# Kernel optimization log

Hardware: AMD Instinct MI355X
Metric: run time of the kernel (lower is better)

The kernel has to match this reference:

```python
import jax, jax.numpy as jnp
import numpy as np

NUM_EXPERT = 8
IN_FEAT = 1024
OUT_FEAT = 1024
N_TOKENS = 8192


def setup_inputs() -> dict:
    key = jax.random.key(0)
    k_inp, k_gate, k_w = jax.random.split(key, 3)
    inp = jax.random.normal(k_inp, (N_TOKENS, IN_FEAT), dtype=jnp.float32)
    gate = jax.random.randint(k_gate, (N_TOKENS,), 0, NUM_EXPERT, dtype=jnp.int32)
    # FMoELinear weight: [num_expert, out_feat, in_feat], kaiming-uniform-like init
    bound = 1.0 / np.sqrt(IN_FEAT)
    weight = jax.random.uniform(
        k_w, (NUM_EXPERT, OUT_FEAT, IN_FEAT), dtype=jnp.float32,
        minval=-bound, maxval=bound)
    return {"inp": inp, "gate": gate, "weight": weight}


def reference(inp, gate, weight):
    # out[i] = weight[gate[i]] @ inp[i]  (top-1 MoE dispatch + grouped GEMM + combine)
    # Loop over the small fixed expert set via scan; each step does a masked
    # dense GEMM so only tokens routed to expert e contribute.
    n, _ = inp.shape
    num_expert, out_feat, _ = weight.shape

    def body(acc, ew):
        e, w_e = ew  # w_e: [out_feat, in_feat]
        mask = (gate == e).astype(inp.dtype)[:, None]  # [n, 1]
        acc = acc + (inp * mask) @ w_e.T               # [n, out_feat]
        return acc, None

    init = jnp.zeros((n, out_feat), dtype=inp.dtype)
    out, _ = jax.lax.scan(body, init, (jnp.arange(num_expert), weight))
    return out
```

## Files before the change

### kernel.cpp

```cpp
#include <hip/hip_runtime.h>
#include <hip/hip_bf16.h>

#define N_TOKENS 8192
#define IN_FEAT 1024
#define OUT_FEAT 1024
#define NUM_EXPERT 8

#define BM 128
#define BN 128
#define BK 32
#define MAXT 71

typedef __bf16 bf16x8 __attribute__((ext_vector_type(8)));
typedef float f32x4 __attribute__((ext_vector_type(4)));

__device__ __forceinline__ unsigned int rne16(float x) {
    union { float f; unsigned int u; } c;
    c.f = x;
    unsigned int u = c.u;
    u += 0x7fffu + ((u >> 16) & 1u);
    return u >> 16;
}
__device__ __forceinline__ unsigned int pk2(float x, float y) {
    return rne16(x) | (rne16(y) << 16);
}

__device__ __forceinline__ void load_lds16(const void* g, void* l) {
    __builtin_amdgcn_global_load_lds(
        (const __attribute__((address_space(1))) unsigned int*)g,
        (__attribute__((address_space(3))) unsigned int*)l,
        16, 0, 0);
}


__global__ __launch_bounds__(256) void moe_hist(const int* __restrict__ gate,
                                                int* __restrict__ cnt) {
    __shared__ int lc[NUM_EXPERT];
    const int t = threadIdx.x;
    if (t < NUM_EXPERT) lc[t] = 0;
    __syncthreads();
    int g = gate[blockIdx.x * 256 + t];
    atomicAdd(&lc[g], 1);
    __syncthreads();
    if (t < NUM_EXPERT) atomicAdd(&cnt[t], lc[t]);
}

__global__ void moe_scan(const int* __restrict__ cnt, int* __restrict__ seg,
                         int* __restrict__ cur, int* __restrict__ tiles,
                         int* __restrict__ ntiles) {
    int s = 0;
    #pragma unroll
    for (int e = 0; e < NUM_EXPERT; ++e) { seg[e] = s; cur[e] = s; s += cnt[e]; }
    seg[NUM_EXPERT] = s;
    int T = 0;
    for (int e = 0; e < NUM_EXPERT; ++e) {
        int c = cnt[e], b = seg[e];
        for (int mt = 0; mt * BM < c; ++mt) {
            int rows = c - mt * BM; if (rows > BM) rows = BM;
            tiles[T++] = (b + mt * BM) | (e << 13) | (rows << 16);
        }
    }
    *ntiles = T;
}

__global__ __launch_bounds__(256) void moe_scatter(const int* __restrict__ gate,
                                                   int* __restrict__ cur,
                                                   int* __restrict__ perm) {
    const int t = threadIdx.x;
    const int lane = t & 63;
    const unsigned long long lt = (lane == 0) ? 0ull : (~0ull >> (64 - lane));
    const int i = blockIdx.x * 256 + t;
    int g = gate[i];
    #pragma unroll
    for (int e = 0; e < NUM_EXPERT; ++e) {
        unsigned long long m = __ballot(g == e);
        if (g == e) {
            int rank = __popcll(m & lt);
            int leader = (int)__ffsll((unsigned long long)m) - 1;
            int p0 = 0;
            if (rank == 0) p0 = atomicAdd(&cur[e], __popcll(m));
            p0 = __shfl(p0, leader);
            perm[p0 + rank] = i;
        }
    }
}

__global__ __launch_bounds__(256) void moe_prep(const float* __restrict__ inp,
                                                const float* __restrict__ weight,
                                                const int* __restrict__ perm,
                                                unsigned int* __restrict__ A2,
                                                unsigned int* __restrict__ W2) {
    const int bid = blockIdx.x;
    const int t = threadIdx.x;
    const int wave = t >> 6, lane = t & 63;
    const float* src;
    unsigned int* dst;
    if (bid < 2048) {
        int row = bid * 4 + wave;
        src = inp + perm[row] * IN_FEAT;
        dst = A2 + row * (IN_FEAT / 2);
    } else {
        int row = (bid - 2048) * 4 + wave;
        src = weight + row * IN_FEAT;
        dst = W2 + row * (IN_FEAT / 2);
    }
    #pragma unroll
    for (int j = 0; j < 4; ++j) {
        float4 v = *(const float4*)(src + j * 256 + lane * 4);
        uint2 o;
        o.x = pk2(v.x, v.y);
        o.y = pk2(v.z, v.w);
        *(uint2*)(dst + j * 128 + lane * 2) = o;
    }
}

__global__ __launch_bounds__(256, 4) void moe_gemm(
    const unsigned short* __restrict__ A2,
    const unsigned short* __restrict__ W2,
    const int* __restrict__ perm,
    const int* __restrict__ tiles,
    const int* __restrict__ ntiles,
    float* __restrict__ out) {

    const int bid = blockIdx.x;
    const int tIdx = bid >> 3;
    const int ntile = bid & 7;
    if (tIdx >= *ntiles) return;
    const int tile = tiles[tIdx];
    const int tbase = tile & 8191;
    const int e = (tile >> 13) & 7;
    const int rows = tile >> 16;

    __shared__ unsigned short lA[2][BM * BK];
    __shared__ unsigned short lB[2][BN * BK];
    __shared__ int rowids[BM];

    const int t = threadIdx.x;
    if (t < BM) {
        int r = tbase + t;
        rowids[t] = perm[r < N_TOKENS ? r : N_TOKENS - 1];
    }

    const int crow = t >> 2;
    const int p = (t & 3) ^ (crow & 3);
    int ar0 = tbase + crow;       if (ar0 > N_TOKENS - 1) ar0 = N_TOKENS - 1;
    int ar1 = tbase + 64 + crow;  if (ar1 > N_TOKENS - 1) ar1 = N_TOKENS - 1;
    const unsigned short* gA0 = A2 + ar0 * IN_FEAT + p * 8;
    const unsigned short* gA1 = A2 + ar1 * IN_FEAT + p * 8;
    const unsigned short* gB0 = W2 + e * (OUT_FEAT * IN_FEAT)
                                + (ntile * BN + crow) * IN_FEAT + p * 8;
    const unsigned short* gB1 = gB0 + 64 * IN_FEAT;
    const int dofs = t * 8;
    const int dofs2 = (t + 256) * 8;

    const int wave = t >> 6;
    const int lane = t & 63;
    const int wm = (wave & 1) << 6;
    const int wn = (wave >> 1) << 6;
    const int l15 = lane & 15;
    const int quad = lane >> 4;
    const int qx = quad ^ (l15 & 3);
    const int fofsA = (wm + l15) * BK + qx * 8;
    const int fofsB = (wn + l15) * BK + qx * 8;

    f32x4 acc[4][4];
    #pragma unroll
    for (int i = 0; i < 4; ++i)
        #pragma unroll
        for (int j = 0; j < 4; ++j)
            acc[i][j] = (f32x4)0.0f;

    load_lds16(gA0, &lA[0][dofs]);
    load_lds16(gA1, &lA[0][dofs2]);
    load_lds16(gB0, &lB[0][dofs]);
    load_lds16(gB1, &lB[0][dofs2]);

    #pragma unroll 1
    for (int kk = 0; kk < 16; ++kk) {
        const int k0 = kk * 64;

        __syncthreads();
        load_lds16(gA0 + k0 + 32, &lA[1][dofs]);
        load_lds16(gA1 + k0 + 32, &lA[1][dofs2]);
        load_lds16(gB0 + k0 + 32, &lB[1][dofs]);
        load_lds16(gB1 + k0 + 32, &lB[1][dofs2]);

        {
            bf16x8 af[4], bq[4];
            #pragma unroll
            for (int i = 0; i < 4; ++i)
                af[i] = *(const bf16x8*)&lA[0][fofsA + i * 16 * BK];
            #pragma unroll
            for (int j = 0; j < 4; ++j)
                bq[j] = *(const bf16x8*)&lB[0][fofsB + j * 16 * BK];
            #pragma unroll
            for (int i = 0; i < 4; ++i)
                #pragma unroll
                for (int j = 0; j < 4; ++j)
                    acc[i][j] = __builtin_amdgcn_mfma_f32_16x16x32_bf16(
                        af[i], bq[j], acc[i][j], 0, 0, 0);
        }

        __syncthreads();
        if (kk < 15) {
            load_lds16(gA0 + k0 + 64, &lA[0][dofs]);
            load_lds16(gA1 + k0 + 64, &lA[0][dofs2]);
            load_lds16(gB0 + k0 + 64, &lB[0][dofs]);
            load_lds16(gB1 + k0 + 64, &lB[0][dofs2]);
        }

        {
            bf16x8 af[4], bq[4];
            #pragma unroll
            for (int i = 0; i < 4; ++i)
                af[i] = *(const bf16x8*)&lA[1][fofsA + i * 16 * BK];
            #pragma unroll
            for (int j = 0; j < 4; ++j)
                bq[j] = *(const bf16x8*)&lB[1][fofsB + j * 16 * BK];
            #pragma unroll
            for (int i = 0; i < 4; ++i)
                #pragma unroll
                for (int j = 0; j < 4; ++j)
                    acc[i][j] = __builtin_amdgcn_mfma_f32_16x16x32_bf16(
                        af[i], bq[j], acc[i][j], 0, 0, 0);
        }
    }

    #pragma unroll
    for (int mi = 0; mi < 4; ++mi) {
        #pragma unroll
        for (int r = 0; r < 4; ++r) {
            int row = wm + mi * 16 + quad * 4 + r;
            if (row < rows) {
                int token = rowids[row];
                float* op = out + token * OUT_FEAT + ntile * BN + wn;
                #pragma unroll
                for (int ni = 0; ni < 4; ++ni)
                    op[ni * 16 + l15] = acc[mi][ni][r];
            }
        }
    }
}

#define FLDSW 20
__global__ __launch_bounds__(256, 4) void moe_gemm_fb(
    const float* __restrict__ inp,
    const float* __restrict__ weight,
    const int* __restrict__ perm,
    const int* __restrict__ seg,
    float* __restrict__ out) {

    const int bid = blockIdx.x;
    const int mtile = bid >> 7;
    const int e = (bid >> 4) & 7;
    const int ntile = bid & 15;

    const int base = seg[e];
    const int cnt = seg[e + 1] - base;
    if (mtile * 128 >= cnt) return;

    __shared__ unsigned int lA[128 * FLDSW];
    __shared__ unsigned int lB[64 * FLDSW];
    __shared__ int rowids[128];

    const int t = threadIdx.x;
    if (t < 128) {
        int r = mtile * 128 + t;
        rowids[t] = (r < cnt) ? perm[base + r] : -1;
    }
    __syncthreads();

    const int srow = t >> 1;
    const int scol = (t & 1) << 4;
    const int tokA = rowids[srow];
    const bool aval = (tokA >= 0);
    const float* aptr = inp + (aval ? tokA : 0) * IN_FEAT + scol;
    const int sdstA = srow * FLDSW + (scol >> 1);
    const int browB = t >> 2;
    const int bcol = (t & 3) << 3;
    const float* bptr = weight + e * (OUT_FEAT * IN_FEAT)
                        + (ntile * 64 + browB) * IN_FEAT + bcol;
    const int sdstB = browB * FLDSW + (bcol >> 1);

    const int wave = t >> 6;
    const int lane = t & 63;
    const int wm = (wave & 1) << 6;
    const int wn = (wave >> 1) << 5;
    const int l15 = lane & 15;
    const int quad = lane >> 4;

    f32x4 acc[4][2];
    #pragma unroll
    for (int i = 0; i < 4; ++i)
        #pragma unroll
        for (int j = 0; j < 2; ++j)
            acc[i][j] = (f32x4)0.0f;

    float4 ra[4], rb[2];
    {
        const float4* ap = (const float4*)aptr;
        const float4* bp = (const float4*)bptr;
        #pragma unroll
        for (int i = 0; i < 4; ++i) ra[i] = ap[i];
        #pragma unroll
        for (int i = 0; i < 2; ++i) rb[i] = bp[i];
    }

    for (int k0 = 0; k0 < IN_FEAT; k0 += 32) {
        unsigned int ua[8], ub[4];
        #pragma unroll
        for (int i = 0; i < 4; ++i) {
            ua[2 * i]     = pk2(ra[i].x, ra[i].y);
            ua[2 * i + 1] = pk2(ra[i].z, ra[i].w);
        }
        #pragma unroll
        for (int i = 0; i < 2; ++i) {
            ub[2 * i]     = pk2(rb[i].x, rb[i].y);
            ub[2 * i + 1] = pk2(rb[i].z, rb[i].w);
        }
        if (!aval) {
            #pragma unroll
            for (int i = 0; i < 8; ++i) ua[i] = 0u;
        }

        __syncthreads();
        *(uint4*)&lA[sdstA]     = make_uint4(ua[0], ua[1], ua[2], ua[3]);
        *(uint4*)&lA[sdstA + 4] = make_uint4(ua[4], ua[5], ua[6], ua[7]);
        *(uint4*)&lB[sdstB]     = make_uint4(ub[0], ub[1], ub[2], ub[3]);
        __syncthreads();

        if (k0 + 32 < IN_FEAT) {
            const float4* ap = (const float4*)(aptr + k0 + 32);
            const float4* bp = (const float4*)(bptr + k0 + 32);
            #pragma unroll
            for (int i = 0; i < 4; ++i) ra[i] = ap[i];
            #pragma unroll
            for (int i = 0; i < 2; ++i) rb[i] = bp[i];
        }

        bf16x8 af[4], bq[2];
        #pragma unroll
        for (int i = 0; i < 4; ++i)
            af[i] = *(const bf16x8*)&lA[(wm + i * 16 + l15) * FLDSW + (quad << 2)];
        #pragma unroll
        for (int j = 0; j < 2; ++j)
            bq[j] = *(const bf16x8*)&lB[(wn + j * 16 + l15) * FLDSW + (quad << 2)];

        #pragma unroll
        for (int i = 0; i < 4; ++i)
            #pragma unroll
            for (int j = 0; j < 2; ++j)
                acc[i][j] = __builtin_amdgcn_mfma_f32_16x16x32_bf16(
                    af[i], bq[j], acc[i][j], 0, 0, 0);
    }

    #pragma unroll
    for (int mi = 0; mi < 4; ++mi) {
        #pragma unroll
        for (int r = 0; r < 4; ++r) {
            int row = wm + mi * 16 + quad * 4 + r;
            int token = rowids[row];
            if (token >= 0) {
                float* op = out + token * OUT_FEAT + ntile * 64 + wn;
                #pragma unroll
                for (int ni = 0; ni < 2; ++ni)
                    op[ni * 16 + l15] = acc[mi][ni][r];
            }
        }
    }
}

extern "C" void kernel_launch(void* const* d_in, const int* in_sizes, int n_in,
                              void* d_out, int out_size, void* d_ws, size_t ws_size,
                              hipStream_t stream) {
    const float* inp = (const float*)d_in[0];
    const int* gate = (const int*)d_in[1];
    const float* weight = (const float*)d_in[2];
    float* out = (float*)d_out;

    int* perm = (int*)d_ws;
    int* seg = perm + N_TOKENS;
    int* cnt = seg + 16;
    int* cur = cnt + 8;
    int* tiles = cur + 8;
    int* ntiles = tiles + 96;

    hipMemsetAsync(cnt, 0, 16 * sizeof(int), stream);
    moe_hist<<<N_TOKENS / 256, 256, 0, stream>>>(gate, cnt);
    moe_scan<<<1, 1, 0, stream>>>(cnt, seg, cur, tiles, ntiles);
    moe_scatter<<<N_TOKENS / 256, 256, 0, stream>>>(gate, cur, perm);

    const size_t need = 65536 + 2ull * N_TOKENS * IN_FEAT * 2;
    if (ws_size >= need) {
        unsigned int* A2 = (unsigned int*)((char*)d_ws + 65536);
        unsigned int* W2 = A2 + (N_TOKENS * IN_FEAT / 2);
        moe_prep<<<4096, 256, 0, stream>>>(inp, weight, perm, A2, W2);
        moe_gemm<<<MAXT * 8, 256, 0, stream>>>((const unsigned short*)A2,
                                               (const unsigned short*)W2,
                                               perm, tiles, ntiles, out);
    } else {
        moe_gemm_fb<<<8192, 256, 0, stream>>>(inp, weight, perm, seg, out);
    }
}
```

Before: 162.0 us.

## Deepen MoE GEMM LDS pipeline to four stages with one barrier per step

Replaces the double-buffered K loop with a four-buffer ring that keeps three tiles of global-to-LDS loads in flight. Each step waits with a partial vmcnt and uses a single barrier instead of two syncthreads. The aim is to hide global load latency and cut synchronisation. LDS use doubles, so launch bounds drop from 4 to 2 blocks per CU. The rowids shared array is removed and tokens are read from perm directly in the epilogue.

```diff
diff --git a/kernel.cpp b/kernel.cpp
--- a/kernel.cpp
+++ b/kernel.cpp
@@ -114,7 +114,7 @@
     }
 }
 
-__global__ __launch_bounds__(256, 4) void moe_gemm(
+__global__ __launch_bounds__(256, 2) void moe_gemm(
     const unsigned short* __restrict__ A2,
     const unsigned short* __restrict__ W2,
     const int* __restrict__ perm,
@@ -131,15 +131,10 @@
     const int e = (tile >> 13) & 7;
     const int rows = tile >> 16;
 
-    __shared__ unsigned short lA[2][BM * BK];
-    __shared__ unsigned short lB[2][BN * BK];
-    __shared__ int rowids[BM];
-
-    const int t = threadIdx.x;
-    if (t < BM) {
-        int r = tbase + t;
-        rowids[t] = perm[r < N_TOKENS ? r : N_TOKENS - 1];
-    }
+    __shared__ __align__(16) unsigned short lA[4][BM * BK];
+    __shared__ __align__(16) unsigned short lB[4][BN * BK];
+
+    const int t = threadIdx.x;
 
     const int crow = t >> 2;
     const int p = (t & 3) ^ (crow & 3);
@@ -170,61 +165,48 @@
         for (int j = 0; j < 4; ++j)
             acc[i][j] = (f32x4)0.0f;
 
-    load_lds16(gA0, &lA[0][dofs]);
-    load_lds16(gA1, &lA[0][dofs2]);
-    load_lds16(gB0, &lB[0][dofs]);
-    load_lds16(gB1, &lB[0][dofs2]);
+#define ISSUE(sidx, buf) do {                                          \
+        int _s = (sidx) > 31 ? 31 : (sidx);                            \
+        load_lds16(gA0 + _s * BK, &lA[buf][dofs]);                     \
+        load_lds16(gA1 + _s * BK, &lA[buf][dofs2]);                    \
+        load_lds16(gB0 + _s * BK, &lB[buf][dofs]);                     \
+        load_lds16(gB1 + _s * BK, &lB[buf][dofs2]);                    \
+    } while (0)
+
+    ISSUE(0, 0);
+    ISSUE(1, 1);
+    ISSUE(2, 2);
+
+#define STAGE(b) {                                                     \
+        const int s = ss * 4 + (b);                                    \
+        asm volatile("s_waitcnt vmcnt(8)" ::: "memory");               \
+        __builtin_amdgcn_s_barrier();                                  \
+        asm volatile("" ::: "memory");                                 \
+        ISSUE(s + 3, ((b) + 3) & 3);                                   \
+        bf16x8 af[4], bq[4];                                           \
+        _Pragma("unroll")                                              \
+        for (int i = 0; i < 4; ++i)                                    \
+            af[i] = *(const bf16x8*)&lA[b][fofsA + i * 16 * BK];       \
+        _Pragma("unroll")                                              \
+        for (int j = 0; j < 4; ++j)                                    \
+            bq[j] = *(const bf16x8*)&lB[b][fofsB + j * 16 * BK];       \
+        _Pragma("unroll")                                              \
+        for (int i = 0; i < 4; ++i)                                    \
+            _Pragma("unroll")                                          \
+            for (int j = 0; j < 4; ++j)                                \
+                acc[i][j] = __builtin_amdgcn_mfma_f32_16x16x32_bf16(   \
+                    af[i], bq[j], acc[i][j], 0, 0, 0);                 \
+    }
 
     #pragma unroll 1
-    for (int kk = 0; kk < 16; ++kk) {
-        const int k0 = kk * 64;
-
-        __syncthreads();
-        load_lds16(gA0 + k0 + 32, &lA[1][dofs]);
-        load_lds16(gA1 + k0 + 32, &lA[1][dofs2]);
-        load_lds16(gB0 + k0 + 32, &lB[1][dofs]);
-        load_lds16(gB1 + k0 + 32, &lB[1][dofs2]);
-
-        {
-            bf16x8 af[4], bq[4];
-            #pragma unroll
-            for (int i = 0; i < 4; ++i)
-                af[i] = *(const bf16x8*)&lA[0][fofsA + i * 16 * BK];
-            #pragma unroll
-            for (int j = 0; j < 4; ++j)
-                bq[j] = *(const bf16x8*)&lB[0][fofsB + j * 16 * BK];
-            #pragma unroll
-            for (int i = 0; i < 4; ++i)
-                #pragma unroll
-                for (int j = 0; j < 4; ++j)
-                    acc[i][j] = __builtin_amdgcn_mfma_f32_16x16x32_bf16(
-                        af[i], bq[j], acc[i][j], 0, 0, 0);
-        }
-
-        __syncthreads();
-        if (kk < 15) {
-            load_lds16(gA0 + k0 + 64, &lA[0][dofs]);
-            load_lds16(gA1 + k0 + 64, &lA[0][dofs2]);
-            load_lds16(gB0 + k0 + 64, &lB[0][dofs]);
-            load_lds16(gB1 + k0 + 64, &lB[0][dofs2]);
-        }
-
-        {
-            bf16x8 af[4], bq[4];
-            #pragma unroll
-            for (int i = 0; i < 4; ++i)
-                af[i] = *(const bf16x8*)&lA[1][fofsA + i * 16 * BK];
-            #pragma unroll
-            for (int j = 0; j < 4; ++j)
-                bq[j] = *(const bf16x8*)&lB[1][fofsB + j * 16 * BK];
-            #pragma unroll
-            for (int i = 0; i < 4; ++i)
-                #pragma unroll
-                for (int j = 0; j < 4; ++j)
-                    acc[i][j] = __builtin_amdgcn_mfma_f32_16x16x32_bf16(
-                        af[i], bq[j], acc[i][j], 0, 0, 0);
-        }
-    }
+    for (int ss = 0; ss < 8; ++ss) {
+        STAGE(0)
+        STAGE(1)
+        STAGE(2)
+        STAGE(3)
+    }
+#undef STAGE
+#undef ISSUE
 
     #pragma unroll
     for (int mi = 0; mi < 4; ++mi) {
@@ -232,7 +214,7 @@
         for (int r = 0; r < 4; ++r) {
             int row = wm + mi * 16 + quad * 4 + r;
             if (row < rows) {
-                int token = rowids[row];
+                int token = perm[tbase + row];
                 float* op = out + token * OUT_FEAT + ntile * BN + wn;
                 #pragma unroll
                 for (int ni = 0; ni < 4; ++ni)
```

Result: slower. 169.7 us (+4.7%).
